# Performance work log

Hardware: AMD Instinct MI355X
Metric: run time of the kernel (lower is better)

Reference implementation:

```python
import jax, jax.numpy as jnp
import numpy as np

D_MODEL = 1024
N_HEAD = 16
D_HEAD = 64


def setup_inputs() -> dict:
    key = jax.random.key(0)
    k1, k2, k3 = jax.random.split(key, 3)
    B, T = 2, 2048
    x = jax.random.normal(k1, (B, T, D_MODEL), dtype=jnp.float32)
    # Linear weights (scaled like typical init to keep softmax numerics sane)
    w_attn = jax.random.normal(k2, (D_MODEL, 3 * D_MODEL), dtype=jnp.float32) * (1.0 / np.sqrt(D_MODEL))
    w_proj = jax.random.normal(k3, (D_MODEL, D_MODEL), dtype=jnp.float32) * (1.0 / np.sqrt(D_MODEL))
    return {"x": x, "w_attn": w_attn, "w_proj": w_proj}


def reference(x, w_attn, w_proj):
    B, T, C = x.shape
    # c_attn: fused qkv projection (use_bias=False)
    qkv = jnp.einsum('btc,cf->btf', x, w_attn)  # [B, T, 3C]
    q, k, v = jnp.split(qkv, 3, axis=-1)
    q = q.reshape(B, T, N_HEAD, D_HEAD)
    k = k.reshape(B, T, N_HEAD, D_HEAD)
    v = v.reshape(B, T, N_HEAD, D_HEAD)
    # scaled QK^T with causal mask (cache=None training path)
    att = jnp.einsum('bqhd,bkhd->bhqk', q, k) * (1.0 / jnp.sqrt(jnp.float32(D_HEAD)))
    causal = jnp.tril(jnp.ones((T, T), dtype=bool))  # [T, T]
    att = jnp.where(causal[None, None, :, :], att, -jnp.inf)
    att = jax.nn.softmax(att, axis=-1)
    # dropout is a no-op (deterministic / p=0)
    y = jnp.einsum('bhqk,bkhd->bqhd', att, v).reshape(B, T, C)
    y = jnp.einsum('btc,cd->btd', y, w_proj)
    return y
```

## Files before the change

kernel.cpp:

```cpp
#include <hip/hip_runtime.h>
#include <hip/hip_bf16.h>


typedef __attribute__((ext_vector_type(8))) __bf16 bf16x8;
typedef __attribute__((ext_vector_type(4))) float  floatx4;
typedef __attribute__((ext_vector_type(4))) float  fvec4;
typedef __attribute__((ext_vector_type(4))) short  short4v;

#define MFMA16(a, b, c) __builtin_amdgcn_mfma_f32_16x16x32_bf16(a, b, c, 0, 0, 0)

using as1v = const __attribute__((address_space(1))) void;
using as3v = __attribute__((address_space(3))) void;
__device__ __forceinline__ void async16(const void* g, void* l) {
  __builtin_amdgcn_global_load_lds((as1v*)g, (as3v*)l, 16, 0, 0);
}

__global__ __launch_bounds__(256) void prep_kernel(const float* __restrict__ x,
                                                   const float* __restrict__ w_attn,
                                                   const float* __restrict__ w_proj,
                                                   __hip_bfloat16* __restrict__ xb,
                                                   __hip_bfloat16* __restrict__ wat,
                                                   __hip_bfloat16* __restrict__ wpt) {
  const int bid = blockIdx.x, tid = threadIdx.x;
  if (bid < 4096) {
    const int i = (bid * 256 + tid) * 4;
    fvec4 v = *(const fvec4*)(x + i);
    union { short4v s; __hip_bfloat16 h[4]; } u;
#pragma unroll
    for (int j = 0; j < 4; ++j) u.h[j] = __float2bfloat16(v[j]);
    *(short4v*)((short*)xb + i) = u.s;
    return;
  }
  __shared__ __align__(16) __hip_bfloat16 tile[64 * 64];
  const float* in;
  __hip_bfloat16* out;
  int cols, bx, by;
  if (bid < 4864) {
    const int b2 = bid - 4096;
    in = w_attn; out = wat; cols = 3072; bx = b2 % 48; by = b2 / 48;
  } else {
    const int b2 = bid - 4864;
    in = w_proj; out = wpt; cols = 1024; bx = b2 % 16; by = b2 / 16;
  }
  const int c0 = bx * 64, r0 = by * 64;
#pragma unroll
  for (int it = 0; it < 2; ++it) {
    const int c = it * 256 + tid;
    const int row = c >> 3, cg = c & 7;
    const float* src = in + (long)(r0 + row) * cols + c0 + cg * 8;
    fvec4 v0 = *(const fvec4*)src;
    fvec4 v1 = *(const fvec4*)(src + 4);
    union { bf16x8 v; __hip_bfloat16 h[8]; } u;
#pragma unroll
    for (int j = 0; j < 4; ++j) { u.h[j] = __float2bfloat16(v0[j]); u.h[4 + j] = __float2bfloat16(v1[j]); }
    *(bf16x8*)(tile + row * 64 + (cg ^ ((row >> 3) & 7)) * 8) = u.v;
  }
  __syncthreads();
#pragma unroll
  for (int it = 0; it < 2; ++it) {
    const int c = it * 256 + tid;
    const int dr = c >> 3, tg = c & 7;
    union { bf16x8 v; __hip_bfloat16 e[8]; } u;
    const int pg = (dr >> 3) ^ tg;
#pragma unroll
    for (int j = 0; j < 8; ++j)
      u.e[j] = tile[(tg * 8 + j) * 64 + pg * 8 + (dr & 7)];
    *(bf16x8*)(out + (long)(c0 + dr) * 1024 + r0 + tg * 8) = u.v;
  }
}

__global__ __launch_bounds__(256) void gemm_qkv_kernel(const __hip_bfloat16* __restrict__ A,
                                                       const __hip_bfloat16* __restrict__ Bt,
                                                       __hip_bfloat16* __restrict__ qk,
                                                       __hip_bfloat16* __restrict__ vt,
                                                       float qscale) {
  const int K = 1024;
  __shared__ __align__(16) __hip_bfloat16 As[2][128 * 32];
  __shared__ __align__(16) __hip_bfloat16 Bs[2][128 * 32];
  const int tid = threadIdx.x;
  const int lane = tid & 63, wv = tid >> 6;
  const int l15 = lane & 15, quad = lane >> 4;
  const int wm = wv >> 1, wn = wv & 1;
  const int wg = blockIdx.x;
  const int i_ = wg >> 3;
  const int by = (wg & 7) * 4 + i_ / 24;
  const int bx = i_ % 24;
  const long m0 = (long)by * 128, n0 = (long)bx * 128;
  floatx4 acc[4][4] = {};
  const int nk = K >> 5;

  auto issue = [&](int kt, int p) {
    const int k0 = kt << 5;
#pragma unroll
    for (int it = 0; it < 2; ++it) {
      const int c = it * 256 + tid;
      const int row = c >> 2;
      const int lcg = (c & 3) ^ ((row >> 1) & 3);
      async16(A + (m0 + row) * K + k0 + lcg * 8, (char*)&As[p][0] + c * 16);
      async16(Bt + (n0 + row) * K + k0 + lcg * 8, (char*)&Bs[p][0] + c * 16);
    }
  };

  issue(0, 0);
  for (int kt = 0; kt < nk; ++kt) {
    const int p = kt & 1;
    __syncthreads();
    if (kt + 1 < nk) issue(kt + 1, p ^ 1);
    bf16x8 af[4], bfr[4];
#pragma unroll
    for (int t = 0; t < 4; ++t) {
      const int ar = wm * 64 + t * 16 + l15;
      const int br = wn * 64 + t * 16 + l15;
      af[t]  = *(const bf16x8*)(&As[p][ar * 32 + (quad ^ ((ar >> 1) & 3)) * 8]);
      bfr[t] = *(const bf16x8*)(&Bs[p][br * 32 + (quad ^ ((br >> 1) & 3)) * 8]);
    }
#pragma unroll
    for (int mt = 0; mt < 4; ++mt)
#pragma unroll
      for (int nt = 0; nt < 4; ++nt)
        acc[mt][nt] = MFMA16(af[mt], bfr[nt], acc[mt][nt]);
  }

#pragma unroll
  for (int nt = 0; nt < 4; ++nt) {
    const int colb = (int)n0 + wn * 64 + nt * 16;
    if (colb >= 2048) {
      const int hh = (colb - 2048) >> 6;
      const int d  = (colb & 63) + l15;
#pragma unroll
      for (int mt = 0; mt < 4; ++mt) {
        const long row = m0 + wm * 64 + mt * 16 + quad * 4;
        const long b   = row >> 11;
        const long t0  = row & 2047;
        union { short4v s; __hip_bfloat16 h[4]; } uy;
#pragma unroll
        for (int r = 0; r < 4; ++r) uy.h[r] = __float2bfloat16(acc[mt][nt][r]);
        *(short4v*)(vt + ((b * 16 + hh) * 64 + d) * 2048 + t0) = uy.s;
      }
    } else {
      const float sc = (colb < 1024) ? qscale : 1.0f;
      const long col = colb + l15;
#pragma unroll
      for (int mt = 0; mt < 4; ++mt)
#pragma unroll
        for (int r = 0; r < 4; ++r) {
          const long row = m0 + wm * 64 + mt * 16 + quad * 4 + r;
          qk[row * 2048 + col] = __float2bfloat16(acc[mt][nt][r] * sc);
        }
    }
  }
}

__global__ __launch_bounds__(256) void gemm_bt64_kernel(const __hip_bfloat16* __restrict__ A,
                                                        const __hip_bfloat16* __restrict__ Bt,
                                                        float* __restrict__ C,
                                                        int M, int N, int K) {
  __shared__ __align__(16) __hip_bfloat16 As[2][128 * 32];
  __shared__ __align__(16) __hip_bfloat16 Bs[2][64 * 32];
  const int tid = threadIdx.x;
  const int lane = tid & 63, wv = tid >> 6;
  const int l15 = lane & 15, quad = lane >> 4;
  const int wm = wv >> 1, wn = wv & 1;
  const long m0 = (long)blockIdx.y * 128, n0 = (long)blockIdx.x * 64;
  floatx4 acc[4][2] = {};
  const int nk = K >> 5;

  auto issue = [&](int kt, int p) {
    const int k0 = kt << 5;
#pragma unroll
    for (int it = 0; it < 2; ++it) {
      const int c = it * 256 + tid;
      const int row = c >> 2;
      const int lcg = (c & 3) ^ ((row >> 1) & 3);
      async16(A + (m0 + row) * K + k0 + lcg * 8, (char*)&As[p][0] + c * 16);
    }
    {
      const int c = tid;
      const int row = c >> 2;
      const int lcg = (c & 3) ^ ((row >> 1) & 3);
      async16(Bt + (n0 + row) * K + k0 + lcg * 8, (char*)&Bs[p][0] + c * 16);
    }
  };

  issue(0, 0);
  for (int kt = 0; kt < nk; ++kt) {
    const int p = kt & 1;
    __syncthreads();
    if (kt + 1 < nk) issue(kt + 1, p ^ 1);
    bf16x8 af[4], bfr[2];
#pragma unroll
    for (int t = 0; t < 4; ++t) {
      const int ar = wm * 64 + t * 16 + l15;
      af[t] = *(const bf16x8*)(&As[p][ar * 32 + (quad ^ ((ar >> 1) & 3)) * 8]);
    }
#pragma unroll
    for (int t = 0; t < 2; ++t) {
      const int br = wn * 32 + t * 16 + l15;
      bfr[t] = *(const bf16x8*)(&Bs[p][br * 32 + (quad ^ ((br >> 1) & 3)) * 8]);
    }
#pragma unroll
    for (int mt = 0; mt < 4; ++mt)
#pragma unroll
      for (int nt = 0; nt < 2; ++nt)
        acc[mt][nt] = MFMA16(af[mt], bfr[nt], acc[mt][nt]);
  }
#pragma unroll
  for (int mt = 0; mt < 4; ++mt)
#pragma unroll
    for (int nt = 0; nt < 2; ++nt)
#pragma unroll
      for (int r = 0; r < 4; ++r) {
        const long row = m0 + wm * 64 + mt * 16 + quad * 4 + r;
        const long col = n0 + wn * 32 + nt * 16 + l15;
        C[row * N + col] = acc[mt][nt][r];
      }
}

__global__ __launch_bounds__(512, 2) void attn_kernel(const __hip_bfloat16* __restrict__ qk,
                                                      const __hip_bfloat16* __restrict__ vtg,
                                                      __hip_bfloat16* __restrict__ y) {
  __shared__ __align__(16) char smem[81920];
  __hip_bfloat16* KsB = (__hip_bfloat16*)smem;
  __hip_bfloat16* VtB = (__hip_bfloat16*)(smem + 32768);
  __hip_bfloat16* PbB = (__hip_bfloat16*)(smem + 65536);

  const int tid = threadIdx.x;
  const int lane = tid & 63, wv = tid >> 6;
  const int l15 = lane & 15, quad = lane >> 4;
  const int g = wv >> 2, sub = wv & 3;
  const int wg = blockIdx.x;
  const int xcd = wg & 7;
  const int r_ = wg >> 3;
  const int pt = r_ & 15;
  const int hb = xcd + 8 * (r_ >> 4);
  const int h = hb & 15, b = hb >> 4;
  const int qtA = pt, qtB = 31 - pt;
  const int q0A = qtA * 64, q0B = qtB * 64;
  const long bh = (long)b * 16 + h;
  const long RS = 2048;

  const int srow = tid >> 3;
  const int scg = (tid & 7) ^ (srow & 7);
  const __hip_bfloat16* kbase = qk + ((long)b * 2048 + srow) * RS + 1024 + h * 64 + scg * 8;
  const __hip_bfloat16* vbase = vtg + (bh * 64 + srow) * 2048 + scg * 8;
  char* ldst = smem + tid * 16;

  auto issue = [&](int pr, int buf) {
#pragma unroll
    for (int par = 0; par < 2; ++par) {
      const int kt = 2 * pr + par;
      if (kt <= qtB) {
        const long kb = (long)kt * 64;
        async16(kbase + kb * RS, ldst + buf * 16384 + par * 8192);
        async16(vbase + kb,      ldst + 32768 + buf * 16384 + par * 8192);
      }
    }
  };

  bf16x8 bqA0, bqA1, bqB0, bqB1;
  {
    const __hip_bfloat16* qpA = qk + ((long)b * 2048 + q0A + sub * 16 + l15) * RS + h * 64 + quad * 8;
    bqA0 = *(const bf16x8*)qpA;
    bqA1 = *(const bf16x8*)(qpA + 32);
    const __hip_bfloat16* qpB = qk + ((long)b * 2048 + q0B + sub * 16 + l15) * RS + h * 64 + quad * 8;
    bqB0 = *(const bf16x8*)qpB;
    bqB1 = *(const bf16x8*)(qpB + 32);
  }
  union { bf16x8 v; __hip_bfloat16 e[8]; } uo;
#pragma unroll
  for (int j = 0; j < 8; ++j) uo.e[j] = __float2bfloat16(1.0f);
  const bf16x8 ones = uo.v;

  floatx4 oA[4] = {}, oB[4] = {}, o4A = {}, o4B = {};
  __hip_bfloat16* Pw = PbB + wv * (16 * 64);
  const int m7 = l15 & 7;

  const int npairs = (qtB + 2) >> 1;
  issue(0, 0);
  for (int pr = 0; pr < npairs; ++pr) {
    const int buf = pr & 1;
    __syncthreads();
    if (pr + 1 < npairs) issue(pr + 1, buf ^ 1);
    const int kt = 2 * pr + g;
    if (kt > qtB) continue;
    const int kb = kt * 64;
    const __hip_bfloat16* Ksp = KsB + buf * 8192 + g * 4096;
    const __hip_bfloat16* Vsp = VtB + buf * 8192 + g * 4096;

    bf16x8 kf[4][2], vf[4][2];
#pragma unroll
    for (int nt = 0; nt < 4; ++nt) {
      const int row = nt * 16 + l15;
      const int s0 = (quad ^ (row & 7)) * 8, s1 = ((quad + 4) ^ (row & 7)) * 8;
      kf[nt][0] = *(const bf16x8*)(&Ksp[row * 64 + s0]);
      kf[nt][1] = *(const bf16x8*)(&Ksp[row * 64 + s1]);
      vf[nt][0] = *(const bf16x8*)(&Vsp[row * 64 + s0]);
      vf[nt][1] = *(const bf16x8*)(&Vsp[row * 64 + s1]);
    }

    auto tile = [&](const bf16x8& bq0, const bf16x8& bq1, floatx4* o, floatx4& o4,
                    bool diag, int q0X) {
      floatx4 st[4] = {};
      __builtin_amdgcn_s_setprio(1);
#pragma unroll
      for (int nt = 0; nt < 4; ++nt) {
        st[nt] = MFMA16(kf[nt][0], bq0, st[nt]);
        st[nt] = MFMA16(kf[nt][1], bq1, st[nt]);
      }
      __builtin_amdgcn_s_setprio(0);
      if (diag) {
        const int qg = q0X + sub * 16 + l15;
#pragma unroll
        for (int nt = 0; nt < 4; ++nt) {
          union { short4v s; __hip_bfloat16 h[4]; } up;
#pragma unroll
          for (int r = 0; r < 4; ++r) {
            float pv = exp2f(st[nt][r]);
            if (kb + nt * 16 + quad * 4 + r > qg) pv = 0.f;
            up.h[r] = __float2bfloat16(pv);
          }
          const int chunk = (nt * 2 + (quad >> 1)) ^ m7;
          *(short4v*)(Pw + l15 * 64 + chunk * 8 + (quad & 1) * 4) = up.s;
        }
      } else {
#pragma unroll
        for (int nt = 0; nt < 4; ++nt) {
          union { short4v s; __hip_bfloat16 h[4]; } up;
#pragma unroll
          for (int r = 0; r < 4; ++r) up.h[r] = __float2bfloat16(exp2f(st[nt][r]));
          const int chunk = (nt * 2 + (quad >> 1)) ^ m7;
          *(short4v*)(Pw + l15 * 64 + chunk * 8 + (quad & 1) * 4) = up.s;
        }
      }
      const bf16x8 pb0 = *(const bf16x8*)(Pw + l15 * 64 + (quad ^ m7) * 8);
      const bf16x8 pb1 = *(const bf16x8*)(Pw + l15 * 64 + ((quad + 4) ^ m7) * 8);
      __builtin_amdgcn_s_setprio(1);
#pragma unroll
      for (int mt = 0; mt < 4; ++mt) {
        o[mt] = MFMA16(vf[mt][0], pb0, o[mt]);
        o[mt] = MFMA16(vf[mt][1], pb1, o[mt]);
      }
      o4 = MFMA16(ones, pb0, o4);
      o4 = MFMA16(ones, pb1, o4);
      __builtin_amdgcn_s_setprio(0);
    };

    tile(bqB0, bqB1, oB, o4B, kt == qtB, q0B);
    if (kt <= qtA) tile(bqA0, bqA1, oA, o4A, kt == qtA, q0A);
  }

  __syncthreads();
  floatx4* redv = (floatx4*)smem;
  if (g == 1) {
#pragma unroll
    for (int mt = 0; mt < 4; ++mt) {
      redv[(sub * 10 + mt) * 64 + lane] = oA[mt];
      redv[(sub * 10 + 4 + mt) * 64 + lane] = oB[mt];
    }
    redv[(sub * 10 + 8) * 64 + lane] = o4A;
    redv[(sub * 10 + 9) * 64 + lane] = o4B;
  }
  __syncthreads();
  if (g == 0) {
#pragma unroll
    for (int mt = 0; mt < 4; ++mt) {
      oA[mt] += redv[(sub * 10 + mt) * 64 + lane];
      oB[mt] += redv[(sub * 10 + 4 + mt) * 64 + lane];
    }
    o4A += redv[(sub * 10 + 8) * 64 + lane];
    o4B += redv[(sub * 10 + 9) * 64 + lane];

    auto epi = [&](floatx4* o, floatx4& o4, int q0X) {
      const float inv = 1.0f / o4[0];
      const long t = (long)b * 2048 + q0X + sub * 16 + l15;
#pragma unroll
      for (int mt = 0; mt < 4; ++mt) {
        union { short4v s; __hip_bfloat16 h[4]; } uy;
#pragma unroll
        for (int r = 0; r < 4; ++r) uy.h[r] = __float2bfloat16(o[mt][r] * inv);
        *(short4v*)(y + t * 1024 + h * 64 + mt * 16 + quad * 4) = uy.s;
      }
    };
    epi(oA, o4A, q0A);
    epi(oB, o4B, q0B);
  }
}

extern "C" void kernel_launch(void* const* d_in, const int* in_sizes, int n_in,
                              void* d_out, int out_size, void* d_ws, size_t ws_size,
                              hipStream_t stream) {
  const float* x      = (const float*)d_in[0];
  const float* w_attn = (const float*)d_in[1];
  const float* w_proj = (const float*)d_in[2];
  float* out = (float*)d_out;
  char* ws = (char*)d_ws;
  __hip_bfloat16* xb  = (__hip_bfloat16*)(ws);
  __hip_bfloat16* wat = (__hip_bfloat16*)(ws + 8388608);
  __hip_bfloat16* qk  = (__hip_bfloat16*)(ws + 16777216);
  __hip_bfloat16* wpt = (__hip_bfloat16*)(ws + 33554432);
  __hip_bfloat16* vtg = (__hip_bfloat16*)(ws + 35651584);
  __hip_bfloat16* yb  = wat;
  const float SC = 0.18033688011112042f;

  prep_kernel<<<5120, 256, 0, stream>>>(x, w_attn, w_proj, xb, wat, wpt);
  gemm_qkv_kernel<<<768, 256, 0, stream>>>(xb, wat, qk, vtg, SC);
  attn_kernel<<<512, 512, 0, stream>>>(qk, vtg, yb);
  gemm_bt64_kernel<<<dim3(16, 32), 256, 0, stream>>>(yb, wpt, out, 4096, 1024, 1024);
}
```

Baseline: 180.5 us.

## Process four K/V tiles per barrier with larger double-buffered LDS chunks

The attention loop now stages four 64-row K/V tiles per iteration, two per wave group, instead of two. This halves the number of __syncthreads and async-load phases across the causal sweep. LDS grows from 80 KB to 144 KB per block, so the two-blocks-per-CU launch bound can no longer be met within the CU's LDS and occupancy likely drops. The s_setprio hints around the MFMA sections are also removed.

```diff
diff --git a/kernel.cpp b/kernel.cpp
--- a/kernel.cpp
+++ b/kernel.cpp
@@ -219,10 +219,8 @@
 __global__ __launch_bounds__(512, 2) void attn_kernel(const __hip_bfloat16* __restrict__ qk,
                                                       const __hip_bfloat16* __restrict__ vtg,
                                                       __hip_bfloat16* __restrict__ y) {
-  __shared__ __align__(16) char smem[81920];
-  __hip_bfloat16* KsB = (__hip_bfloat16*)smem;
-  __hip_bfloat16* VtB = (__hip_bfloat16*)(smem + 32768);
-  __hip_bfloat16* PbB = (__hip_bfloat16*)(smem + 65536);
+  __shared__ __align__(16) char smem[147456];
+  __hip_bfloat16* PbB = (__hip_bfloat16*)(smem + 131072);
 
   const int tid = threadIdx.x;
   const int lane = tid & 63, wv = tid >> 6;
@@ -245,16 +243,19 @@
   const __hip_bfloat16* vbase = vtg + (bh * 64 + srow) * 2048 + scg * 8;
   char* ldst = smem + tid * 16;
 
-  auto issue = [&](int pr, int buf) {
-#pragma unroll
-    for (int par = 0; par < 2; ++par) {
-      const int kt = 2 * pr + par;
-      if (kt <= qtB) {
-        const long kb = (long)kt * 64;
-        async16(kbase + kb * RS, ldst + buf * 16384 + par * 8192);
-        async16(vbase + kb,      ldst + 32768 + buf * 16384 + par * 8192);
+  auto issue = [&](int ch, int buf) {
+#pragma unroll
+    for (int g2 = 0; g2 < 2; ++g2)
+#pragma unroll
+      for (int sb = 0; sb < 2; ++sb) {
+        const int kt = 4 * ch + 2 * g2 + sb;
+        if (kt <= qtB) {
+          const long kb = (long)kt * 64;
+          const int off = buf * 32768 + g2 * 16384 + sb * 8192;
+          async16(kbase + kb * RS, ldst + off);
+          async16(vbase + kb, ldst + 65536 + off);
+        }
       }
-    }
   };
 
   bf16x8 bqA0, bqA1, bqB0, bqB1;
@@ -275,78 +276,79 @@
   __hip_bfloat16* Pw = PbB + wv * (16 * 64);
   const int m7 = l15 & 7;
 
-  const int npairs = (qtB + 2) >> 1;
+  const int nch = (qtB >> 2) + 1;
   issue(0, 0);
-  for (int pr = 0; pr < npairs; ++pr) {
-    const int buf = pr & 1;
+  for (int ch = 0; ch < nch; ++ch) {
+    const int buf = ch & 1;
     __syncthreads();
-    if (pr + 1 < npairs) issue(pr + 1, buf ^ 1);
-    const int kt = 2 * pr + g;
-    if (kt > qtB) continue;
-    const int kb = kt * 64;
-    const __hip_bfloat16* Ksp = KsB + buf * 8192 + g * 4096;
-    const __hip_bfloat16* Vsp = VtB + buf * 8192 + g * 4096;
-
-    bf16x8 kf[4][2], vf[4][2];
-#pragma unroll
-    for (int nt = 0; nt < 4; ++nt) {
-      const int row = nt * 16 + l15;
-      const int s0 = (quad ^ (row & 7)) * 8, s1 = ((quad + 4) ^ (row & 7)) * 8;
-      kf[nt][0] = *(const bf16x8*)(&Ksp[row * 64 + s0]);
-      kf[nt][1] = *(const bf16x8*)(&Ksp[row * 64 + s1]);
-      vf[nt][0] = *(const bf16x8*)(&Vsp[row * 64 + s0]);
-      vf[nt][1] = *(const bf16x8*)(&Vsp[row * 64 + s1]);
-    }
-
-    auto tile = [&](const bf16x8& bq0, const bf16x8& bq1, floatx4* o, floatx4& o4,
-                    bool diag, int q0X) {
-      floatx4 st[4] = {};
-      __builtin_amdgcn_s_setprio(1);
+    if (ch + 1 < nch) issue(ch + 1, buf ^ 1);
+
+#pragma unroll
+    for (int sb = 0; sb < 2; ++sb) {
+      const int kt = 4 * ch + 2 * g + sb;
+      if (kt > qtB) continue;
+      const int kb = kt * 64;
+      const int off = buf * 32768 + g * 16384 + sb * 8192;
+      const __hip_bfloat16* Ksp = (const __hip_bfloat16*)(smem + off);
+      const __hip_bfloat16* Vsp = (const __hip_bfloat16*)(smem + 65536 + off);
+
+      bf16x8 kf[4][2], vf[4][2];
 #pragma unroll
       for (int nt = 0; nt < 4; ++nt) {
-        st[nt] = MFMA16(kf[nt][0], bq0, st[nt]);
-        st[nt] = MFMA16(kf[nt][1], bq1, st[nt]);
+        const int row = nt * 16 + l15;
+        const int s0 = (quad ^ (row & 7)) * 8, s1 = ((quad + 4) ^ (row & 7)) * 8;
+        kf[nt][0] = *(const bf16x8*)(&Ksp[row * 64 + s0]);
+        kf[nt][1] = *(const bf16x8*)(&Ksp[row * 64 + s1]);
+        vf[nt][0] = *(const bf16x8*)(&Vsp[row * 64 + s0]);
+        vf[nt][1] = *(const bf16x8*)(&Vsp[row * 64 + s1]);
       }
-      __builtin_amdgcn_s_setprio(0);
-      if (diag) {
-        const int qg = q0X + sub * 16 + l15;
+
+      auto tile = [&](const bf16x8& bq0, const bf16x8& bq1, floatx4* o, floatx4& o4,
+                      bool diag, int q0X) {
+        floatx4 st[4] = {};
 #pragma unroll
         for (int nt = 0; nt < 4; ++nt) {
-          union { short4v s; __hip_bfloat16 h[4]; } up;
-#pragma unroll
-          for (int r = 0; r < 4; ++r) {
-            float pv = exp2f(st[nt][r]);
-            if (kb + nt * 16 + quad * 4 + r > qg) pv = 0.f;
-            up.h[r] = __float2bfloat16(pv);
+          st[nt] = MFMA16(kf[nt][0], bq0, st[nt]);
+          st[nt] = MFMA16(kf[nt][1], bq1, st[nt]);
+        }
+        if (diag) {
+          const int qg = q0X + sub * 16 + l15;
+#pragma unroll
+          for (int nt = 0; nt < 4; ++nt) {
+            union { short4v s; __hip_bfloat16 h[4]; } up;
+#pragma unroll
+            for (int r = 0; r < 4; ++r) {
+              float pv = exp2f(st[nt][r]);
+              if (kb + nt * 16 + quad * 4 + r > qg) pv = 0.f;
+              up.h[r] = __float2bfloat16(pv);
+            }
+            const int chunk = (nt * 2 + (quad >> 1)) ^ m7;
+            *(short4v*)(Pw + l15 * 64 + chunk * 8 + (quad & 1) * 4) = up.s;
           }
-          const int chunk = (nt * 2 + (quad >> 1)) ^ m7;
-          *(short4v*)(Pw + l15 * 64 + chunk * 8 + (quad & 1) * 4) = up.s;
+        } else {
+#pragma unroll
+          for (int nt = 0; nt < 4; ++nt) {
+            union { short4v s; __hip_bfloat16 h[4]; } up;
+#pragma unroll
+            for (int r = 0; r < 4; ++r) up.h[r] = __float2bfloat16(exp2f(st[nt][r]));
+            const int chunk = (nt * 2 + (quad >> 1)) ^ m7;
+            *(short4v*)(Pw + l15 * 64 + chunk * 8 + (quad & 1) * 4) = up.s;
+          }
         }
-      } else {
-#pragma unroll
-        for (int nt = 0; nt < 4; ++nt) {
-          union { short4v s; __hip_bfloat16 h[4]; } up;
-#pragma unroll
-          for (int r = 0; r < 4; ++r) up.h[r] = __float2bfloat16(exp2f(st[nt][r]));
-          const int chunk = (nt * 2 + (quad >> 1)) ^ m7;
-          *(short4v*)(Pw + l15 * 64 + chunk * 8 + (quad & 1) * 4) = up.s;
+        const bf16x8 pb0 = *(const bf16x8*)(Pw + l15 * 64 + (quad ^ m7) * 8);
+        const bf16x8 pb1 = *(const bf16x8*)(Pw + l15 * 64 + ((quad + 4) ^ m7) * 8);
+#pragma unroll
+        for (int mt = 0; mt < 4; ++mt) {
+          o[mt] = MFMA16(vf[mt][0], pb0, o[mt]);
+          o[mt] = MFMA16(vf[mt][1], pb1, o[mt]);
         }
-      }
-      const bf16x8 pb0 = *(const bf16x8*)(Pw + l15 * 64 + (quad ^ m7) * 8);
-      const bf16x8 pb1 = *(const bf16x8*)(Pw + l15 * 64 + ((quad + 4) ^ m7) * 8);
-      __builtin_amdgcn_s_setprio(1);
-#pragma unroll
-      for (int mt = 0; mt < 4; ++mt) {
-        o[mt] = MFMA16(vf[mt][0], pb0, o[mt]);
-        o[mt] = MFMA16(vf[mt][1], pb1, o[mt]);
-      }
-      o4 = MFMA16(ones, pb0, o4);
-      o4 = MFMA16(ones, pb1, o4);
-      __builtin_amdgcn_s_setprio(0);
-    };
-
-    tile(bqB0, bqB1, oB, o4B, kt == qtB, q0B);
-    if (kt <= qtA) tile(bqA0, bqA1, oA, o4A, kt == qtA, q0A);
+        o4 = MFMA16(ones, pb0, o4);
+        o4 = MFMA16(ones, pb1, o4);
+      };
+
+      tile(bqB0, bqB1, oB, o4B, kt == qtB, q0B);
+      if (kt <= qtA) tile(bqA0, bqA1, oA, o4A, kt == qtA, q0A);
+    }
   }
 
   __syncthreads();
```

After: 181.5 us. Within noise of the previous version (+0.6%).
